# Optimization experiments

Hardware: AMD Instinct MI355X
Metric: run time of the kernel (lower is better)

Reference implementation:

```python
import jax, jax.numpy as jnp
import numpy as np

NUM_SHAPES, NUM_COLORS, NUM_CLASSES = 8, 8, 10
HID = 64
N_NODES, N_EDGES, N_REL, N_GRAPHS = 100000, 1600000, 3, 1024


def setup_inputs() -> dict:
    key = jax.random.key(0)
    ks = jax.random.split(key, 16)
    f = jnp.float32
    inp = {
        "x_idx": jax.random.randint(ks[0], (N_NODES, 2), 0, NUM_SHAPES),
        "edge_index": jax.random.randint(ks[1], (2, N_EDGES), 0, N_NODES),
        "edge_type": jax.random.randint(ks[2], (N_EDGES,), 0, N_REL),
        "batch": jnp.sort(jax.random.randint(ks[3], (N_NODES,), 0, N_GRAPHS)),
        # parameters (Linear weights stored as [in, out])
        "shape_emb": jax.random.normal(ks[4], (NUM_SHAPES, 8), f),
        "color_emb": jax.random.normal(ks[5], (NUM_COLORS, 8), f),
        "lin0_w": jax.random.normal(ks[6], (16, HID), f) * 0.1,
        "lin0_b": jnp.zeros((HID,), f),
        "r1_wrel": jax.random.normal(ks[7], (N_REL, HID, HID), f) * 0.05,
        "r1_wroot": jax.random.normal(ks[8], (HID, HID), f) * 0.05,
        "r1_b": jnp.zeros((HID,), f),
        "r2_wrel": jax.random.normal(ks[9], (N_REL, HID, HID), f) * 0.05,
        "r2_wroot": jax.random.normal(ks[10], (HID, HID), f) * 0.05,
        "r2_b": jnp.zeros((HID,), f),
        "cls_w": jax.random.normal(ks[11], (HID, NUM_CLASSES), f) * 0.1,
        "cls_b": jnp.zeros((NUM_CLASSES,), f),
    }
    return inp


def _rgcn(x, edge_index, edge_type, w_rel, w_root, b):
    # PyG RGCNConv with aggr='mean': per-relation mean of transformed neighbors + root + bias
    n = x.shape[0]
    xw = jnp.einsum('nd,rde->rne', x, w_rel)            # [R, N, H] (cheap dense)
    src, dst = edge_index[0], edge_index[1]
    msg = xw[edge_type, src]                            # [E, H] gather
    seg = edge_type * n + dst                           # combined (relation, node) segment id
    sums = jax.ops.segment_sum(msg, seg, num_segments=N_REL * n)
    cnt = jax.ops.segment_sum(jnp.ones_like(seg, dtype=x.dtype), seg, num_segments=N_REL * n)
    mean = sums / jnp.maximum(cnt, 1.0)[:, None]
    agg = mean.reshape(N_REL, n, -1).sum(axis=0)        # sum over relations
    return agg + x @ w_root + b


def reference(x_idx, edge_index, edge_type, batch,
              shape_emb, color_emb, lin0_w, lin0_b,
              r1_wrel, r1_wroot, r1_b, r2_wrel, r2_wroot, r2_b,
              cls_w, cls_b):
    x = jnp.concatenate([shape_emb[x_idx[:, 0]], color_emb[x_idx[:, 1]]], axis=1)  # [N, 16]
    x = jax.nn.relu(x @ lin0_w + lin0_b)
    x = jax.nn.relu(_rgcn(x, edge_index, edge_type, r1_wrel, r1_wroot, r1_b))
    x = jax.nn.relu(_rgcn(x, edge_index, edge_type, r2_wrel, r2_wroot, r2_b))
    # global mean pool over graphs
    sums = jax.ops.segment_sum(x, batch, num_segments=N_GRAPHS)
    cnt = jax.ops.segment_sum(jnp.ones((x.shape[0],), x.dtype), batch, num_segments=N_GRAPHS)
    pooled = sums / jnp.maximum(cnt, 1.0)[:, None]
    return pooled @ cls_w + cls_b
```

## Files before the change

### kernel.cpp

```cpp
#include <hip/hip_runtime.h>

#define NN 100000
#define NE 1600000
#define NRL 3
#define NG 1024
#define NBUCK 782
#define NXCD 8
#define PSTRIDE 384
#define BSLOTS (NXCD * PSTRIDE)
#define NKEY 384
#define OSTRIDE 392
#define EB 4096

typedef __attribute__((ext_vector_type(8))) short bf16x8;
typedef __attribute__((ext_vector_type(4))) float f32x4;
typedef __attribute__((ext_vector_type(2))) float f32x2;

__device__ __forceinline__ int xcd_id() {
    unsigned int x;
    asm volatile("s_getreg_b32 %0, hwreg(HW_REG_XCC_ID)" : "=s"(x));
    return (int)(x & 7);
}

__device__ __forceinline__ unsigned short f2bf(float f) {
    unsigned u = __float_as_uint(f);
    unsigned r = (u + 0x7fffu + ((u >> 16) & 1u)) >> 16;
    return (unsigned short)r;
}

__global__ void k_embed(const int* __restrict__ x_idx,
                        const float* __restrict__ semb, const float* __restrict__ cemb,
                        const float* __restrict__ w, const float* __restrict__ b,
                        unsigned short* __restrict__ xbf) {
    __shared__ float s_w[16 * 64];
    __shared__ float s_se[64], s_ce[64], s_b[64];
    int t = threadIdx.x;
    for (int i = t; i < 16 * 64; i += 256) s_w[i] = w[i];
    if (t < 64) { s_se[t] = semb[t]; s_ce[t] = cemb[t]; s_b[t] = b[t]; }
    __syncthreads();
    int gid = blockIdx.x * 256 + t;
    int v = gid >> 6, h = gid & 63;
    int si = x_idx[2 * v], ci = x_idx[2 * v + 1];
    float acc = s_b[h];
#pragma unroll
    for (int d = 0; d < 8; ++d) acc += s_se[si * 8 + d] * s_w[d * 64 + h];
#pragma unroll
    for (int d = 0; d < 8; ++d) acc += s_ce[ci * 8 + d] * s_w[(8 + d) * 64 + h];
    xbf[gid] = f2bf(fmaxf(acc, 0.f));
}

__global__ __launch_bounds__(256) void k_bucket(
        const int* __restrict__ ei, const int* __restrict__ et,
        int* __restrict__ bcnt, unsigned int* __restrict__ arena) {
    __shared__ unsigned int   s_srt[EB];
    __shared__ unsigned short s_skey[EB];
    __shared__ int s_hist[NBUCK], s_start[NBUCK + 1], s_base[NBUCK], s_pos[NBUCK];
    int t = threadIdx.x;
    int e0 = blockIdx.x * EB;
    int n = NE - e0; if (n > EB) n = EB;
    int p = xcd_id();

    for (int i = t; i < NBUCK; i += 256) s_hist[i] = 0;
    __syncthreads();

    for (int i = t; i < n; i += 256) {
        int dst = __builtin_nontemporal_load(ei + NE + e0 + i);
        atomicAdd(&s_hist[dst >> 7], 1);
    }
    __syncthreads();
    if (t == 0) {
        int run = 0;
#pragma unroll 8
        for (int k = 0; k < NBUCK; ++k) { s_start[k] = run; run += s_hist[k]; }
        s_start[NBUCK] = run;
    }
    __syncthreads();
    for (int k = t; k < NBUCK; k += 256) {
        s_pos[k] = s_start[k];
        s_base[k] = (s_hist[k] > 0) ? atomicAdd(&bcnt[k * NXCD + p], s_hist[k]) : 0;
    }
    __syncthreads();

    for (int i = t; i < n; i += 256) {
        int e = e0 + i;
        int src = __builtin_nontemporal_load(ei + e);
        int dst = __builtin_nontemporal_load(ei + NE + e);
        int rel = __builtin_nontemporal_load(et + e);
        int key = dst >> 7;
        unsigned int rec = (unsigned int)src | ((unsigned int)rel << 17) |
                           ((unsigned int)(dst & 127) << 19);
        int q = atomicAdd(&s_pos[key], 1);
        s_srt[q] = rec;
        s_skey[q] = (unsigned short)key;
    }
    __syncthreads();

    for (int i = t; i < n; i += 256) {
        int key = (int)s_skey[i];
        int off = s_base[key] + (i - s_start[key]);
        if (off < PSTRIDE)
            arena[((size_t)key * NXCD + p) * PSTRIDE + off] = s_srt[i];
    }
}

__global__ __launch_bounds__(256) void k_sortbucket(
        const int* __restrict__ bcnt, unsigned int* __restrict__ arena,
        unsigned short* __restrict__ off16) {
    __shared__ unsigned int s_rec[BSLOTS];
    __shared__ unsigned int s_srt[BSLOTS];
    __shared__ int s_hist[NKEY + 1], s_start[NKEY + 1], s_pos[NKEY];
    int t = threadIdx.x;
    int b = blockIdx.x;

    for (int i = t; i < NKEY + 1; i += 256) s_hist[i] = 0;
    __syncthreads();

    int tot = 0;
#pragma unroll
    for (int p = 0; p < NXCD; ++p) {
        int c = bcnt[b * NXCD + p]; if (c > PSTRIDE) c = PSTRIDE;
        const unsigned int* src = arena + ((size_t)(b * NXCD + p)) * PSTRIDE;
        for (int i = t; i < c; i += 256) {
            unsigned int r = __builtin_nontemporal_load(src + i);
            s_rec[tot + i] = r;
            int key = ((r >> 19) & 127) * 3 + ((r >> 17) & 3);
            atomicAdd(&s_hist[key], 1);
        }
        tot += c;
    }
    __syncthreads();
    if (t == 0) {
        int run = 0;
#pragma unroll 8
        for (int k = 0; k < NKEY; ++k) { s_start[k] = run; run += s_hist[k]; }
        s_start[NKEY] = run;
    }
    __syncthreads();
    for (int i = t; i < NKEY; i += 256) s_pos[i] = s_start[i];
    __syncthreads();
    for (int i = t; i < tot; i += 256) {
        unsigned int r = s_rec[i];
        int key = ((r >> 19) & 127) * 3 + ((r >> 17) & 3);
        int p = atomicAdd(&s_pos[key], 1);
        s_srt[p] = (r & 0x1FFFF) << 7;
    }
    __syncthreads();
    for (int i = t; i < tot; i += 256)
        arena[(size_t)b * BSLOTS + i] = s_srt[i];
    for (int i = t; i < NKEY + 1; i += 256)
        off16[(size_t)b * OSTRIDE + i] = (unsigned short)s_start[i];
}

__global__ void k_agg(const unsigned short* __restrict__ xbf,
                      const unsigned int* __restrict__ arena,
                      const unsigned short* __restrict__ off16,
                      unsigned short* __restrict__ K) {
    int wid = (blockIdx.x * 256 + threadIdx.x) >> 6;
    int lane = threadIdx.x & 63;
    if (wid >= NN) return;
    int v = wid;
    int b = v >> 7, dlo = v & 127;
    const unsigned short* ofs = off16 + (size_t)b * OSTRIDE + dlo * 3;
    int s0 = __builtin_amdgcn_readfirstlane((int)ofs[0]);
    int s1 = __builtin_amdgcn_readfirstlane((int)ofs[1]);
    int s2 = __builtin_amdgcn_readfirstlane((int)ofs[2]);
    int s3 = __builtin_amdgcn_readfirstlane((int)ofs[3]);
    const unsigned int* base = arena + (size_t)b * BSLOTS;

    int g = lane >> 4, sl = lane & 15;
    const char* xpb = (const char*)xbf + 8 * sl;

    f32x2 aT0 = {0.f, 0.f}, aT1 = {0.f, 0.f};
    f32x2 a10 = {0.f, 0.f}, a11 = {0.f, 0.f};
    f32x2 a20 = {0.f, 0.f}, a21 = {0.f, 0.f};
    const f32x2 z = {0.f, 0.f};

    int e = s0;
    for (; e + 8 <= s3; e += 8) {
#pragma unroll
        for (int k = 0; k < 2; ++k) {
            int ee = e + 4 * k + g;
            unsigned off = base[ee];
            uint2 u = *reinterpret_cast<const uint2*>(xpb + off);
            f32x2 f0, f1;
            f0.x = __uint_as_float(u.x << 16);
            f0.y = __uint_as_float(u.x & 0xFFFF0000u);
            f1.x = __uint_as_float(u.y << 16);
            f1.y = __uint_as_float(u.y & 0xFFFF0000u);
            aT0 += f0;  aT1 += f1;
            bool c2 = ee >= s2;
            bool c1 = (ee >= s1) && !c2;
            a10 += c1 ? f0 : z;  a11 += c1 ? f1 : z;
            a20 += c2 ? f0 : z;  a21 += c2 ? f1 : z;
        }
    }
    for (; e < s3; e += 4) {
        int ee = e + g;
        bool ok = ee < s3;
        unsigned off = base[ok ? ee : s3 - 1];
        uint2 u = *reinterpret_cast<const uint2*>(xpb + off);
        if (!ok) { u.x = 0u; u.y = 0u; }
        f32x2 f0, f1;
        f0.x = __uint_as_float(u.x << 16);
        f0.y = __uint_as_float(u.x & 0xFFFF0000u);
        f1.x = __uint_as_float(u.y << 16);
        f1.y = __uint_as_float(u.y & 0xFFFF0000u);
        aT0 += f0;  aT1 += f1;
        bool c2 = ok && (ee >= s2);
        bool c1 = ok && (ee >= s1) && (ee < s2);
        a10 += c1 ? f0 : z;  a11 += c1 ? f1 : z;
        a20 += c2 ? f0 : z;  a21 += c2 ? f1 : z;
    }

#define RED1(V) { V.x += __shfl_xor(V.x, 16); V.y += __shfl_xor(V.y, 16); }
#define RED2(V) { V.x += __shfl_xor(V.x, 32); V.y += __shfl_xor(V.y, 32); }
    RED1(aT0) RED1(aT1) RED1(a10) RED1(a11) RED1(a20) RED1(a21)
    RED2(aT0) RED2(aT1) RED2(a10) RED2(a11) RED2(a20) RED2(a21)
#undef RED1
#undef RED2

    unsigned short* Kv = K + (size_t)v * 256;
    if (lane < 16) {
        f32x2 b00, b01;
        b00.x = aT0.x - a10.x - a20.x;  b00.y = aT0.y - a10.y - a20.y;
        b01.x = aT1.x - a11.x - a21.x;  b01.y = aT1.y - a11.y - a21.y;
        float i0 = 1.f / fmaxf((float)(s1 - s0), 1.f);
        float i1 = 1.f / fmaxf((float)(s2 - s1), 1.f);
        float i2 = 1.f / fmaxf((float)(s3 - s2), 1.f);
        uint2 p0, p1, p2;
        p0.x = (unsigned)f2bf(b00.x * i0) | ((unsigned)f2bf(b00.y * i0) << 16);
        p0.y = (unsigned)f2bf(b01.x * i0) | ((unsigned)f2bf(b01.y * i0) << 16);
        p1.x = (unsigned)f2bf(a10.x * i1) | ((unsigned)f2bf(a10.y * i1) << 16);
        p1.y = (unsigned)f2bf(a11.x * i1) | ((unsigned)f2bf(a11.y * i1) << 16);
        p2.x = (unsigned)f2bf(a20.x * i2) | ((unsigned)f2bf(a20.y * i2) << 16);
        p2.y = (unsigned)f2bf(a21.x * i2) | ((unsigned)f2bf(a21.y * i2) << 16);
        uint2* Kw = reinterpret_cast<uint2*>(Kv);
        Kw[sl]      = p0;
        Kw[16 + sl] = p1;
        Kw[32 + sl] = p2;
    }
    Kv[192 + lane] = xbf[(size_t)v * 64 + lane];
}

__global__ __launch_bounds__(512, 4) void k_transform(
        const unsigned short* __restrict__ K, const float* __restrict__ wrel,
        const float* __restrict__ wroot, const float* __restrict__ b,
        float* __restrict__ xout, unsigned short* __restrict__ xbf) {
    __shared__ __align__(16) unsigned short s_bf[4][8][64][8];
    __shared__ float s_b[64];
    int t = threadIdx.x;
    for (int i = t; i < 4 * 8 * 64 * 8; i += 512) {
        int j  = i & 7;
        int l  = (i >> 3) & 63;
        int c  = (i >> 9) & 7;
        int nt = (i >> 12) & 3;
        int k  = c * 32 + (l >> 4) * 8 + j;
        int n  = nt * 16 + (l & 15);
        const float* src = (k < 192) ? (wrel + k * 64 + n) : (wroot + (k - 192) * 64 + n);
        s_bf[nt][c][l][j] = f2bf(*src);
    }
    if (t < 64) s_b[t] = b[t];
    __syncthreads();

    int wave = t >> 6, lane = t & 63;
    int strip = blockIdx.x * 8 + wave;
    if (strip > NN / 16 - 1) strip = NN / 16 - 1;
    int v0 = strip * 16;

    const unsigned short* Ka = K + (size_t)(v0 + (lane & 15)) * 256 + (lane >> 4) * 8;

    f32x4 acc0 = {0.f, 0.f, 0.f, 0.f};
    f32x4 acc1 = {0.f, 0.f, 0.f, 0.f};
    f32x4 acc2 = {0.f, 0.f, 0.f, 0.f};
    f32x4 acc3 = {0.f, 0.f, 0.f, 0.f};

#pragma unroll
    for (int c = 0; c < 8; ++c) {
        bf16x8 a = *reinterpret_cast<const bf16x8*>(Ka + c * 32);
        bf16x8 b0 = *reinterpret_cast<const bf16x8*>(&s_bf[0][c][lane][0]);
        bf16x8 b1 = *reinterpret_cast<const bf16x8*>(&s_bf[1][c][lane][0]);
        bf16x8 b2 = *reinterpret_cast<const bf16x8*>(&s_bf[2][c][lane][0]);
        bf16x8 b3 = *reinterpret_cast<const bf16x8*>(&s_bf[3][c][lane][0]);
        acc0 = __builtin_amdgcn_mfma_f32_16x16x32_bf16(a, b0, acc0, 0, 0, 0);
        acc1 = __builtin_amdgcn_mfma_f32_16x16x32_bf16(a, b1, acc1, 0, 0, 0);
        acc2 = __builtin_amdgcn_mfma_f32_16x16x32_bf16(a, b2, acc2, 0, 0, 0);
        acc3 = __builtin_amdgcn_mfma_f32_16x16x32_bf16(a, b3, acc3, 0, 0, 0);
    }

    int col = lane & 15, rg = (lane >> 4) * 4;
#pragma unroll
    for (int r = 0; r < 4; ++r) {
        float o0 = fmaxf(acc0[r] + s_b[0  + col], 0.f);
        float o1 = fmaxf(acc1[r] + s_b[16 + col], 0.f);
        float o2 = fmaxf(acc2[r] + s_b[32 + col], 0.f);
        float o3 = fmaxf(acc3[r] + s_b[48 + col], 0.f);
        if (xout) {
            float* op = xout + (size_t)(v0 + rg + r) * 64;
            op[0  + col] = o0;
            op[16 + col] = o1;
            op[32 + col] = o2;
            op[48 + col] = o3;
        }
        if (xbf) {
            unsigned short* ob = xbf + (size_t)(v0 + rg + r) * 64;
            ob[0  + col] = f2bf(o0);
            ob[16 + col] = f2bf(o1);
            ob[32 + col] = f2bf(o2);
            ob[48 + col] = f2bf(o3);
        }
    }
}

#define POOL_CHUNK 32
__global__ void k_pool(const float* __restrict__ x, const int* __restrict__ batch,
                       float* __restrict__ psum, int* __restrict__ pcnt) {
    int gwid = (blockIdx.x * 256 + threadIdx.x) >> 6;
    int lane = threadIdx.x & 63;
    int v0 = gwid * POOL_CHUNK;
    if (v0 >= NN) return;
    int v1 = v0 + POOL_CHUNK; if (v1 > NN) v1 = NN;
    float acc = 0.f;
    int cnt = 0;
    int gcur = batch[v0];
    for (int v = v0; v < v1; ++v) {
        int g = batch[v];
        if (g != gcur) {
            atomicAdd(&psum[gcur * 64 + lane], acc);
            if (lane == 0) atomicAdd(&pcnt[gcur], cnt);
            acc = 0.f; cnt = 0; gcur = g;
        }
        acc += x[(size_t)v * 64 + lane];
        ++cnt;
    }
    atomicAdd(&psum[gcur * 64 + lane], acc);
    if (lane == 0) atomicAdd(&pcnt[gcur], cnt);
}

__global__ void k_cls(const float* __restrict__ psum, const int* __restrict__ pcnt,
                      const float* __restrict__ w, const float* __restrict__ b,
                      float* __restrict__ out) {
    int gid = blockIdx.x * 256 + threadIdx.x;
    if (gid >= NG * 10) return;
    int g = gid / 10, c = gid % 10;
    float inv = 1.f / fmaxf((float)pcnt[g], 1.f);
    float acc = 0.f;
#pragma unroll
    for (int d = 0; d < 64; ++d) acc += psum[g * 64 + d] * w[d * 10 + c];
    out[gid] = acc * inv + b[c];
}

extern "C" void kernel_launch(void* const* d_in, const int* in_sizes, int n_in,
                              void* d_out, int out_size, void* d_ws, size_t ws_size,
                              hipStream_t stream) {
    const int*   x_idx  = (const int*)d_in[0];
    const int*   ei     = (const int*)d_in[1];
    const int*   et     = (const int*)d_in[2];
    const int*   batch  = (const int*)d_in[3];
    const float* semb   = (const float*)d_in[4];
    const float* cemb   = (const float*)d_in[5];
    const float* lin0w  = (const float*)d_in[6];
    const float* lin0b  = (const float*)d_in[7];
    const float* r1wrel = (const float*)d_in[8];
    const float* r1wroot= (const float*)d_in[9];
    const float* r1b    = (const float*)d_in[10];
    const float* r2wrel = (const float*)d_in[11];
    const float* r2wroot= (const float*)d_in[12];
    const float* r2b    = (const float*)d_in[13];
    const float* clsw   = (const float*)d_in[14];
    const float* clsb   = (const float*)d_in[15];
    float* out = (float*)d_out;

    char* ws = (char*)d_ws;
    size_t o = 0;
    auto alloc = [&](size_t bytes) -> void* {
        void* p = ws + o;
        o += (bytes + 255) & ~(size_t)255;
        return p;
    };
    int*            bcnt  = (int*)           alloc((size_t)NBUCK * NXCD * 4);
    unsigned int*   arena = (unsigned int*)  alloc((size_t)NBUCK * BSLOTS * 4);
    unsigned short* off16 = (unsigned short*)alloc((size_t)NBUCK * OSTRIDE * 2);
    float*          xA    = (float*)         alloc((size_t)NN * 64 * 4);
    unsigned short* xbf   = (unsigned short*)alloc((size_t)NN * 64 * 2);
    unsigned short* Kbuf  = (unsigned short*)alloc((size_t)NN * 256 * 2);
    float*          psum  = (float*)         alloc((size_t)NG * 64 * 4);
    int*            pcnt  = (int*)           alloc((size_t)NG * 4);

    hipMemsetAsync(bcnt, 0, (size_t)NBUCK * NXCD * 4, stream);
    hipMemsetAsync(psum, 0, (size_t)NG * 64 * 4, stream);
    hipMemsetAsync(pcnt, 0, (size_t)NG * 4, stream);

    k_embed<<<NN * 64 / 256, 256, 0, stream>>>(x_idx, semb, cemb, lin0w, lin0b, xbf);

    k_bucket<<<(NE + EB - 1) / EB, 256, 0, stream>>>(ei, et, bcnt, arena);
    k_sortbucket<<<NBUCK, 256, 0, stream>>>(bcnt, arena, off16);

    k_agg<<<NN / 4, 256, 0, stream>>>(xbf, arena, off16, Kbuf);
    k_transform<<<(NN / 16 + 7) / 8, 512, 0, stream>>>(Kbuf, r1wrel, r1wroot, r1b,
                                                       (float*)nullptr, xbf);
    k_agg<<<NN / 4, 256, 0, stream>>>(xbf, arena, off16, Kbuf);
    k_transform<<<(NN / 16 + 7) / 8, 512, 0, stream>>>(Kbuf, r2wrel, r2wroot, r2b, xA,
                                                       (unsigned short*)nullptr);

    {
        int nwaves = (NN + POOL_CHUNK - 1) / POOL_CHUNK;
        int nblk = (nwaves * 64 + 255) / 256;
        k_pool<<<nblk, 256, 0, stream>>>(xA, batch, psum, pcnt);
    }
    k_cls<<<(NG * 10 + 255) / 256, 256, 0, stream>>>(psum, pcnt, clsw, clsb, out);
}
```

Before: 284.5 us.

## Fuse neighbor aggregation and MFMA transform into one kernel via shared memory

Merges k_agg and k_transform into k_aggxform. Each 512-thread block aggregates 32 nodes into an LDS K tile and then runs the bf16 MFMA transform from LDS, so the 256-wide bf16 K buffer no longer round-trips through global memory. A second bf16 activation buffer replaces in-place writes, since blocks now read neighbors while others write outputs. In exchange, every block re-converts the full weight matrix into LDS, which is costlier per node than the old 128-node blocks and also cuts occupancy. Each wave now issues one MFMA chain instead of four.

```diff
diff --git a/kernel.cpp b/kernel.cpp
--- a/kernel.cpp
+++ b/kernel.cpp
@@ -11,6 +11,8 @@
 #define NKEY 384
 #define OSTRIDE 392
 #define EB 4096
+#define NB 32
+#define KST 264
 
 typedef __attribute__((ext_vector_type(8))) short bf16x8;
 typedef __attribute__((ext_vector_type(4))) float f32x4;
@@ -151,101 +153,14 @@
         off16[(size_t)b * OSTRIDE + i] = (unsigned short)s_start[i];
 }
 
-__global__ void k_agg(const unsigned short* __restrict__ xbf,
-                      const unsigned int* __restrict__ arena,
-                      const unsigned short* __restrict__ off16,
-                      unsigned short* __restrict__ K) {
-    int wid = (blockIdx.x * 256 + threadIdx.x) >> 6;
-    int lane = threadIdx.x & 63;
-    if (wid >= NN) return;
-    int v = wid;
-    int b = v >> 7, dlo = v & 127;
-    const unsigned short* ofs = off16 + (size_t)b * OSTRIDE + dlo * 3;
-    int s0 = __builtin_amdgcn_readfirstlane((int)ofs[0]);
-    int s1 = __builtin_amdgcn_readfirstlane((int)ofs[1]);
-    int s2 = __builtin_amdgcn_readfirstlane((int)ofs[2]);
-    int s3 = __builtin_amdgcn_readfirstlane((int)ofs[3]);
-    const unsigned int* base = arena + (size_t)b * BSLOTS;
-
-    int g = lane >> 4, sl = lane & 15;
-    const char* xpb = (const char*)xbf + 8 * sl;
-
-    f32x2 aT0 = {0.f, 0.f}, aT1 = {0.f, 0.f};
-    f32x2 a10 = {0.f, 0.f}, a11 = {0.f, 0.f};
-    f32x2 a20 = {0.f, 0.f}, a21 = {0.f, 0.f};
-    const f32x2 z = {0.f, 0.f};
-
-    int e = s0;
-    for (; e + 8 <= s3; e += 8) {
-#pragma unroll
-        for (int k = 0; k < 2; ++k) {
-            int ee = e + 4 * k + g;
-            unsigned off = base[ee];
-            uint2 u = *reinterpret_cast<const uint2*>(xpb + off);
-            f32x2 f0, f1;
-            f0.x = __uint_as_float(u.x << 16);
-            f0.y = __uint_as_float(u.x & 0xFFFF0000u);
-            f1.x = __uint_as_float(u.y << 16);
-            f1.y = __uint_as_float(u.y & 0xFFFF0000u);
-            aT0 += f0;  aT1 += f1;
-            bool c2 = ee >= s2;
-            bool c1 = (ee >= s1) && !c2;
-            a10 += c1 ? f0 : z;  a11 += c1 ? f1 : z;
-            a20 += c2 ? f0 : z;  a21 += c2 ? f1 : z;
-        }
-    }
-    for (; e < s3; e += 4) {
-        int ee = e + g;
-        bool ok = ee < s3;
-        unsigned off = base[ok ? ee : s3 - 1];
-        uint2 u = *reinterpret_cast<const uint2*>(xpb + off);
-        if (!ok) { u.x = 0u; u.y = 0u; }
-        f32x2 f0, f1;
-        f0.x = __uint_as_float(u.x << 16);
-        f0.y = __uint_as_float(u.x & 0xFFFF0000u);
-        f1.x = __uint_as_float(u.y << 16);
-        f1.y = __uint_as_float(u.y & 0xFFFF0000u);
-        aT0 += f0;  aT1 += f1;
-        bool c2 = ok && (ee >= s2);
-        bool c1 = ok && (ee >= s1) && (ee < s2);
-        a10 += c1 ? f0 : z;  a11 += c1 ? f1 : z;
-        a20 += c2 ? f0 : z;  a21 += c2 ? f1 : z;
-    }
-
-#define RED1(V) { V.x += __shfl_xor(V.x, 16); V.y += __shfl_xor(V.y, 16); }
-#define RED2(V) { V.x += __shfl_xor(V.x, 32); V.y += __shfl_xor(V.y, 32); }
-    RED1(aT0) RED1(aT1) RED1(a10) RED1(a11) RED1(a20) RED1(a21)
-    RED2(aT0) RED2(aT1) RED2(a10) RED2(a11) RED2(a20) RED2(a21)
-#undef RED1
-#undef RED2
-
-    unsigned short* Kv = K + (size_t)v * 256;
-    if (lane < 16) {
-        f32x2 b00, b01;
-        b00.x = aT0.x - a10.x - a20.x;  b00.y = aT0.y - a10.y - a20.y;
-        b01.x = aT1.x - a11.x - a21.x;  b01.y = aT1.y - a11.y - a21.y;
-        float i0 = 1.f / fmaxf((float)(s1 - s0), 1.f);
-        float i1 = 1.f / fmaxf((float)(s2 - s1), 1.f);
-        float i2 = 1.f / fmaxf((float)(s3 - s2), 1.f);
-        uint2 p0, p1, p2;
-        p0.x = (unsigned)f2bf(b00.x * i0) | ((unsigned)f2bf(b00.y * i0) << 16);
-        p0.y = (unsigned)f2bf(b01.x * i0) | ((unsigned)f2bf(b01.y * i0) << 16);
-        p1.x = (unsigned)f2bf(a10.x * i1) | ((unsigned)f2bf(a10.y * i1) << 16);
-        p1.y = (unsigned)f2bf(a11.x * i1) | ((unsigned)f2bf(a11.y * i1) << 16);
-        p2.x = (unsigned)f2bf(a20.x * i2) | ((unsigned)f2bf(a20.y * i2) << 16);
-        p2.y = (unsigned)f2bf(a21.x * i2) | ((unsigned)f2bf(a21.y * i2) << 16);
-        uint2* Kw = reinterpret_cast<uint2*>(Kv);
-        Kw[sl]      = p0;
-        Kw[16 + sl] = p1;
-        Kw[32 + sl] = p2;
-    }
-    Kv[192 + lane] = xbf[(size_t)v * 64 + lane];
-}
-
-__global__ __launch_bounds__(512, 4) void k_transform(
-        const unsigned short* __restrict__ K, const float* __restrict__ wrel,
-        const float* __restrict__ wroot, const float* __restrict__ b,
-        float* __restrict__ xout, unsigned short* __restrict__ xbf) {
+__global__ __launch_bounds__(512) void k_aggxform(
+        const unsigned short* __restrict__ xbf,
+        const unsigned int* __restrict__ arena,
+        const unsigned short* __restrict__ off16,
+        const float* __restrict__ wrel, const float* __restrict__ wroot,
+        const float* __restrict__ bias,
+        float* __restrict__ xout, unsigned short* __restrict__ xbfo) {
+    __shared__ __align__(16) unsigned short s_k[NB * KST];
     __shared__ __align__(16) unsigned short s_bf[4][8][64][8];
     __shared__ float s_b[64];
     int t = threadIdx.x;
@@ -259,55 +174,114 @@
         const float* src = (k < 192) ? (wrel + k * 64 + n) : (wroot + (k - 192) * 64 + n);
         s_bf[nt][c][l][j] = f2bf(*src);
     }
-    if (t < 64) s_b[t] = b[t];
-    __syncthreads();
+    if (t < 64) s_b[t] = bias[t];
 
     int wave = t >> 6, lane = t & 63;
-    int strip = blockIdx.x * 8 + wave;
-    if (strip > NN / 16 - 1) strip = NN / 16 - 1;
-    int v0 = strip * 16;
-
-    const unsigned short* Ka = K + (size_t)(v0 + (lane & 15)) * 256 + (lane >> 4) * 8;
-
-    f32x4 acc0 = {0.f, 0.f, 0.f, 0.f};
-    f32x4 acc1 = {0.f, 0.f, 0.f, 0.f};
-    f32x4 acc2 = {0.f, 0.f, 0.f, 0.f};
-    f32x4 acc3 = {0.f, 0.f, 0.f, 0.f};
-
+    int v0 = blockIdx.x * NB;
+    int g = lane >> 4, sl = lane & 15;
+    const char* xpb = (const char*)xbf + 8 * sl;
+
+    for (int i = 0; i < 4; ++i) {
+        int lr = wave * 4 + i;
+        int v = v0 + lr;
+        int b = v >> 7, dlo = v & 127;
+        const unsigned short* ofs = off16 + (size_t)b * OSTRIDE + dlo * 3;
+        int s0 = __builtin_amdgcn_readfirstlane((int)ofs[0]);
+        int s1 = __builtin_amdgcn_readfirstlane((int)ofs[1]);
+        int s2 = __builtin_amdgcn_readfirstlane((int)ofs[2]);
+        int s3 = __builtin_amdgcn_readfirstlane((int)ofs[3]);
+        const unsigned int* base = arena + (size_t)b * BSLOTS;
+
+        f32x2 aT0 = {0.f, 0.f}, aT1 = {0.f, 0.f};
+        f32x2 a10 = {0.f, 0.f}, a11 = {0.f, 0.f};
+        f32x2 a20 = {0.f, 0.f}, a21 = {0.f, 0.f};
+        const f32x2 z = {0.f, 0.f};
+
+        int e = s0;
+        for (; e + 8 <= s3; e += 8) {
+#pragma unroll
+            for (int k = 0; k < 2; ++k) {
+                int ee = e + 4 * k + g;
+                unsigned off = base[ee];
+                uint2 u = *reinterpret_cast<const uint2*>(xpb + off);
+                f32x2 f0, f1;
+                f0.x = __uint_as_float(u.x << 16);
+                f0.y = __uint_as_float(u.x & 0xFFFF0000u);
+                f1.x = __uint_as_float(u.y << 16);
+                f1.y = __uint_as_float(u.y & 0xFFFF0000u);
+                aT0 += f0;  aT1 += f1;
+                bool c2 = ee >= s2;
+                bool c1 = (ee >= s1) && !c2;
+                a10 += c1 ? f0 : z;  a11 += c1 ? f1 : z;
+                a20 += c2 ? f0 : z;  a21 += c2 ? f1 : z;
+            }
+        }
+        for (; e < s3; e += 4) {
+            int ee = e + g;
+            bool ok = ee < s3;
+            unsigned off = base[ok ? ee : s3 - 1];
+            uint2 u = *reinterpret_cast<const uint2*>(xpb + off);
+            if (!ok) { u.x = 0u; u.y = 0u; }
+            f32x2 f0, f1;
+            f0.x = __uint_as_float(u.x << 16);
+            f0.y = __uint_as_float(u.x & 0xFFFF0000u);
+            f1.x = __uint_as_float(u.y << 16);
+            f1.y = __uint_as_float(u.y & 0xFFFF0000u);
+            aT0 += f0;  aT1 += f1;
+            bool c2 = ok && (ee >= s2);
+            bool c1 = ok && (ee >= s1) && (ee < s2);
+            a10 += c1 ? f0 : z;  a11 += c1 ? f1 : z;
+            a20 += c2 ? f0 : z;  a21 += c2 ? f1 : z;
+        }
+
+#define RED1(V) { V.x += __shfl_xor(V.x, 16); V.y += __shfl_xor(V.y, 16); }
+#define RED2(V) { V.x += __shfl_xor(V.x, 32); V.y += __shfl_xor(V.y, 32); }
+        RED1(aT0) RED1(aT1) RED1(a10) RED1(a11) RED1(a20) RED1(a21)
+        RED2(aT0) RED2(aT1) RED2(a10) RED2(a11) RED2(a20) RED2(a21)
+#undef RED1
+#undef RED2
+
+        unsigned short* Kv = s_k + lr * KST;
+        if (lane < 16) {
+            f32x2 b00, b01;
+            b00.x = aT0.x - a10.x - a20.x;  b00.y = aT0.y - a10.y - a20.y;
+            b01.x = aT1.x - a11.x - a21.x;  b01.y = aT1.y - a11.y - a21.y;
+            float i0 = 1.f / fmaxf((float)(s1 - s0), 1.f);
+            float i1 = 1.f / fmaxf((float)(s2 - s1), 1.f);
+            float i2 = 1.f / fmaxf((float)(s3 - s2), 1.f);
+            uint2 p0, p1, p2;
+            p0.x = (unsigned)f2bf(b00.x * i0) | ((unsigned)f2bf(b00.y * i0) << 16);
+            p0.y = (unsigned)f2bf(b01.x * i0) | ((unsigned)f2bf(b01.y * i0) << 16);
+            p1.x = (unsigned)f2bf(a10.x * i1) | ((unsigned)f2bf(a10.y * i1) << 16);
+            p1.y = (unsigned)f2bf(a11.x * i1) | ((unsigned)f2bf(a11.y * i1) << 16);
+            p2.x = (unsigned)f2bf(a20.x * i2) | ((unsigned)f2bf(a20.y * i2) << 16);
+            p2.y = (unsigned)f2bf(a21.x * i2) | ((unsigned)f2bf(a21.y * i2) << 16);
+            uint2* Kw = reinterpret_cast<uint2*>(Kv);
+            Kw[sl]      = p0;
+            Kw[16 + sl] = p1;
+            Kw[32 + sl] = p2;
+        }
+        Kv[192 + lane] = xbf[(size_t)v * 64 + lane];
+    }
+    __syncthreads();
+
+    int sidx = wave >> 2, nt = wave & 3;
+    const unsigned short* Ka = s_k + (size_t)(sidx * 16 + (lane & 15)) * KST
+                                   + (lane >> 4) * 8;
+    f32x4 acc = {0.f, 0.f, 0.f, 0.f};
 #pragma unroll
     for (int c = 0; c < 8; ++c) {
         bf16x8 a = *reinterpret_cast<const bf16x8*>(Ka + c * 32);
-        bf16x8 b0 = *reinterpret_cast<const bf16x8*>(&s_bf[0][c][lane][0]);
-        bf16x8 b1 = *reinterpret_cast<const bf16x8*>(&s_bf[1][c][lane][0]);
-        bf16x8 b2 = *reinterpret_cast<const bf16x8*>(&s_bf[2][c][lane][0]);
-        bf16x8 b3 = *reinterpret_cast<const bf16x8*>(&s_bf[3][c][lane][0]);
-        acc0 = __builtin_amdgcn_mfma_f32_16x16x32_bf16(a, b0, acc0, 0, 0, 0);
-        acc1 = __builtin_amdgcn_mfma_f32_16x16x32_bf16(a, b1, acc1, 0, 0, 0);
-        acc2 = __builtin_amdgcn_mfma_f32_16x16x32_bf16(a, b2, acc2, 0, 0, 0);
-        acc3 = __builtin_amdgcn_mfma_f32_16x16x32_bf16(a, b3, acc3, 0, 0, 0);
-    }
-
+        bf16x8 bb = *reinterpret_cast<const bf16x8*>(&s_bf[nt][c][lane][0]);
+        acc = __builtin_amdgcn_mfma_f32_16x16x32_bf16(a, bb, acc, 0, 0, 0);
+    }
     int col = lane & 15, rg = (lane >> 4) * 4;
 #pragma unroll
     for (int r = 0; r < 4; ++r) {
-        float o0 = fmaxf(acc0[r] + s_b[0  + col], 0.f);
-        float o1 = fmaxf(acc1[r] + s_b[16 + col], 0.f);
-        float o2 = fmaxf(acc2[r] + s_b[32 + col], 0.f);
-        float o3 = fmaxf(acc3[r] + s_b[48 + col], 0.f);
-        if (xout) {
-            float* op = xout + (size_t)(v0 + rg + r) * 64;
-            op[0  + col] = o0;
-            op[16 + col] = o1;
-            op[32 + col] = o2;
-            op[48 + col] = o3;
-        }
-        if (xbf) {
-            unsigned short* ob = xbf + (size_t)(v0 + rg + r) * 64;
-            ob[0  + col] = f2bf(o0);
-            ob[16 + col] = f2bf(o1);
-            ob[32 + col] = f2bf(o2);
-            ob[48 + col] = f2bf(o3);
-        }
+        float o = fmaxf(acc[r] + s_b[nt * 16 + col], 0.f);
+        size_t row = (size_t)(v0 + sidx * 16 + rg + r);
+        if (xout) xout[row * 64 + nt * 16 + col] = o;
+        if (xbfo) xbfo[row * 64 + nt * 16 + col] = f2bf(o);
     }
 }
 
@@ -382,7 +356,7 @@
     unsigned short* off16 = (unsigned short*)alloc((size_t)NBUCK * OSTRIDE * 2);
     float*          xA    = (float*)         alloc((size_t)NN * 64 * 4);
     unsigned short* xbf   = (unsigned short*)alloc((size_t)NN * 64 * 2);
-    unsigned short* Kbuf  = (unsigned short*)alloc((size_t)NN * 256 * 2);
+    unsigned short* xbf2  = (unsigned short*)alloc((size_t)NN * 64 * 2);
     float*          psum  = (float*)         alloc((size_t)NG * 64 * 4);
     int*            pcnt  = (int*)           alloc((size_t)NG * 4);
 
@@ -395,12 +369,10 @@
     k_bucket<<<(NE + EB - 1) / EB, 256, 0, stream>>>(ei, et, bcnt, arena);
     k_sortbucket<<<NBUCK, 256, 0, stream>>>(bcnt, arena, off16);
 
-    k_agg<<<NN / 4, 256, 0, stream>>>(xbf, arena, off16, Kbuf);
-    k_transform<<<(NN / 16 + 7) / 8, 512, 0, stream>>>(Kbuf, r1wrel, r1wroot, r1b,
-                                                       (float*)nullptr, xbf);
-    k_agg<<<NN / 4, 256, 0, stream>>>(xbf, arena, off16, Kbuf);
-    k_transform<<<(NN / 16 + 7) / 8, 512, 0, stream>>>(Kbuf, r2wrel, r2wroot, r2b, xA,
-                                                       (unsigned short*)nullptr);
+    k_aggxform<<<NN / NB, 512, 0, stream>>>(xbf, arena, off16, r1wrel, r1wroot, r1b,
+                                            (float*)nullptr, xbf2);
+    k_aggxform<<<NN / NB, 512, 0, stream>>>(xbf2, arena, off16, r2wrel, r2wroot, r2b,
+                                            xA, (unsigned short*)nullptr);
 
     {
         int nwaves = (NN + POOL_CHUNK - 1) / POOL_CHUNK;
```

Result: slower. 333.5 us (+17.2%).
